# Kernel tuning notes

Hardware: AMD Instinct MI355X
Metric: run time of the kernel (lower is better)

The kernel has to match this reference:

```python
import jax, jax.numpy as jnp
import numpy as np

DIM = 64  # QK head dim, matches init kwarg 'dim'

def setup_inputs() -> dict:
    key = jax.random.key(0)
    kq, kk, kv = jax.random.split(key, 3)
    B, L, C, D, H = 2, 2048, 16, DIM, 64
    query = jax.random.normal(kq, (B, L, C, D), dtype=jnp.float32)
    k_ = jax.random.normal(kk, (B, L, C, D), dtype=jnp.float32)
    value = jax.random.normal(kv, (B, L, C, H), dtype=jnp.float32)
    return {"query": query, "key": k_, "value": value}

def reference(query, key, value):
    scaler = 1.0 / jnp.sqrt(jnp.float32(DIM))
    # score: [b, c, l, m]
    score = jnp.einsum('blcd,bmcd->bclm', query, key) * scaler
    # mask=False, dropout=0 -> identity
    attn = jax.nn.softmax(score, axis=3)
    # out: [b, l, c, h]
    out = jnp.einsum('bmch,bclm->blch', value, attn)
    return out
```

## Files before the change

### kernel.cpp

```cpp
#include <hip/hip_runtime.h>
#include <hip/hip_bf16.h>
#include <stdint.h>

#define B_ 2
#define L_ 2048
#define C_ 16
#define D_ 64
#define H_ 64
#define QBLK 128
#define KVBLK 64
#define NTILES 32
#define NTHREADS 256
#define NHEADS 32
#define TILE_ELEMS 4096
#define TENSOR_ELEMS (NHEADS * NTILES * TILE_ELEMS)

typedef __attribute__((ext_vector_type(8))) short bf16x8;
typedef __attribute__((ext_vector_type(16))) float f32x16;
typedef __attribute__((ext_vector_type(8))) unsigned short u16x8;

__device__ inline unsigned short f2bf(float f) {
  union { float f; unsigned int u; } v; v.f = f;
  unsigned int u = v.u;
  unsigned int r = (u + 0x7FFFu + ((u >> 16) & 1u)) >> 16;
  return (unsigned short)r;
}

__device__ inline float fast_exp2(float x) {
#if __has_builtin(__builtin_amdgcn_exp2f)
  return __builtin_amdgcn_exp2f(x);
#else
  return exp2f(x);
#endif
}

__device__ inline unsigned cvt_pk_bf16(float lo, float hi) {
  unsigned r;
  asm("v_cvt_pk_bf16_f32 %0, %1, %2" : "=v"(r) : "v"(lo), "v"(hi));
  return r;
}

__device__ inline void pl32swap(unsigned &x, unsigned &y) {
#if __has_builtin(__builtin_amdgcn_permlane32_swap)
  auto r = __builtin_amdgcn_permlane32_swap(x, y, false, false);
  x = r[0]; y = r[1];
#else
  asm("v_permlane32_swap_b32 %0, %1" : "+v"(x), "+&v"(y));
#endif
}

__device__ inline float xsum32(float v) {
  unsigned x = __float_as_uint(v), y = x;
  pl32swap(x, y);
  return __uint_as_float(x) + __uint_as_float(y);
}

__global__ __launch_bounds__(256) void prepack_kernel(
    const float* __restrict__ Kg, const float* __restrict__ Vg,
    unsigned short* __restrict__ Kb, unsigned short* __restrict__ Vb) {
  int idx = blockIdx.x * 256 + threadIdx.x;
  if (idx < 524288) {
    int i = idx;
    int lane = i & 63, frag = (i >> 6) & 7, t = (i >> 9) & 31, head = i >> 14;
    int b = head >> 4, c = head & 15;
    int ks = frag >> 1, half = frag & 1;
    int row = half * 32 + (lane & 31);
    int kb = ks * 16 + (lane >> 5) * 8;
    const float* src = Kg + ((size_t)(b * L_ + t * 64 + row) * C_ + c) * D_ + kb;
    float4 a0 = ((const float4*)src)[0];
    float4 a1 = ((const float4*)src)[1];
    u16x8 pk;
    pk[0] = f2bf(a0.x); pk[1] = f2bf(a0.y); pk[2] = f2bf(a0.z); pk[3] = f2bf(a0.w);
    pk[4] = f2bf(a1.x); pk[5] = f2bf(a1.y); pk[6] = f2bf(a1.z); pk[7] = f2bf(a1.w);
    size_t dst = ((((size_t)(head * 32 + t)) * 8 + frag) * 64 + lane) * 8;
    *(u16x8*)&Kb[dst] = pk;
  } else {
    int i = idx - 524288;
    int lane = i & 63, frag = (i >> 6) & 7, t = (i >> 9) & 31, head = i >> 14;
    int b = head >> 4, c = head & 15;
    int m = frag >> 1, half = frag & 1;
    int h = half * 32 + (lane & 31);
    int kv0 = m * 16 + (lane >> 5) * 8;
    const float* src = Vg + ((size_t)(b * L_ + t * 64 + kv0) * C_ + c) * H_ + h;
    u16x8 pv;
#pragma unroll
    for (int j = 0; j < 8; ++j) pv[j] = f2bf(src[(size_t)j * C_ * H_]);
    size_t dst = ((((size_t)(head * 32 + t)) * 8 + frag) * 64 + lane) * 8;
    *(u16x8*)&Vb[dst] = pv;
  }
}

#define TILE_BODY(SC0, SC1, SN0, SN1, T)                                          \
  {                                                                               \
    _Pragma("unroll")                                                             \
    for (int z = 0; z < 16; ++z) { SN0[z] = 0.f; SN1[z] = 0.f; }                  \
    float rst[4];                                                                 \
    bf16x8 pf[4];                                                                 \
    _Pragma("unroll")                                                             \
    for (int i = 0; i < 4; ++i) {                                                 \
      const int be = ((2 * i) & 3) * 4;                                           \
      const int bo = ((2 * i + 1) & 3) * 4;                                       \
      float p0[4], p1[4];                                                         \
      _Pragma("unroll")                                                           \
      for (int r = 0; r < 4; ++r) {                                               \
        float se = (i < 2) ? SC0[be + r] : SC1[be + r];                           \
        float so_ = (i < 2) ? SC0[bo + r] : SC1[bo + r];                          \
        p0[r] = fast_exp2(se);                                                    \
        p1[r] = fast_exp2(so_);                                                   \
      }                                                                           \
      rst[i] = ((p0[0] + p0[1]) + (p0[2] + p0[3])) +                              \
               ((p1[0] + p1[1]) + (p1[2] + p1[3]));                               \
      unsigned x0 = cvt_pk_bf16(p0[0], p0[1]);                                    \
      unsigned x1 = cvt_pk_bf16(p0[2], p0[3]);                                    \
      unsigned y0 = cvt_pk_bf16(p1[0], p1[1]);                                    \
      unsigned y1 = cvt_pk_bf16(p1[2], p1[3]);                                    \
      pl32swap(x0, y0);                                                           \
      pl32swap(x1, y1);                                                           \
      union { unsigned wd[4]; bf16x8 v; } pk_;                                    \
      pk_.wd[0] = x0; pk_.wd[1] = x1; pk_.wd[2] = y0; pk_.wd[3] = y1;             \
      pf[i] = pk_.v;                                                              \
      SN0 = __builtin_amdgcn_mfma_f32_32x32x16_bf16(kf[2 * i], qf[i], SN0, 0, 0, 0);     \
      SN1 = __builtin_amdgcn_mfma_f32_32x32x16_bf16(kf[2 * i + 1], qf[i], SN1, 0, 0, 0); \
    }                                                                             \
    l_own += (rst[0] + rst[1]) + (rst[2] + rst[3]);                               \
    {                                                                             \
      const int tk = ((T) + 2 < NTILES) ? (T) + 2 : NTILES - 1;                   \
      _Pragma("unroll")                                                           \
      for (int f = 0; f < 8; ++f)                                                 \
        kf[f] = *(const bf16x8*)(KbL + (size_t)(tk * 8 + f) * 512);               \
    }                                                                             \
    __builtin_amdgcn_s_setprio(1);                                                \
    _Pragma("unroll")                                                             \
    for (int m = 0; m < 4; ++m) {                                                 \
      o0 = __builtin_amdgcn_mfma_f32_32x32x16_bf16(vf[2 * m], pf[m], o0, 0, 0, 0);       \
      o1 = __builtin_amdgcn_mfma_f32_32x32x16_bf16(vf[2 * m + 1], pf[m], o1, 0, 0, 0);   \
    }                                                                             \
    __builtin_amdgcn_s_setprio(0);                                                \
    {                                                                             \
      const int tv = ((T) + 1 < NTILES) ? (T) + 1 : NTILES - 1;                   \
      _Pragma("unroll")                                                           \
      for (int f = 0; f < 8; ++f)                                                 \
        vf[f] = *(const bf16x8*)(VbL + (size_t)(tv * 8 + f) * 512);               \
    }                                                                             \
  }

__global__ __launch_bounds__(NTHREADS, 2) void attn_fwd_kernel(
    const float* __restrict__ Qg,
    const unsigned short* __restrict__ Kb,
    const unsigned short* __restrict__ Vb,
    float* __restrict__ Og) {
  const int tid  = threadIdx.x;
  const int lane = tid & 63;
  const int w    = tid >> 6;
  const int ql   = lane & 31;
  const int u    = lane >> 5;

  const int bid   = blockIdx.x;
  const int swz   = (bid & 7) * 64 + (bid >> 3);
  const int head  = swz >> 4;
  const int qtile = swz & 15;
  const int b     = head >> 4;
  const int c     = head & 15;
  const int q0    = qtile * QBLK;

  const unsigned short* KbL = Kb + (size_t)head * NTILES * TILE_ELEMS + lane * 8;
  const unsigned short* VbL = Vb + (size_t)head * NTILES * TILE_ELEMS + lane * 8;

  const float sc2 = 0.125f * 1.44269504088896340736f;
  const int qr = q0 + w * 32 + ql;
  const float* qrow = Qg + ((size_t)(b * L_ + qr) * C_ + c) * D_;
  bf16x8 qf[4];
#pragma unroll
  for (int ks = 0; ks < 4; ++ks) {
    float4 a0 = *(const float4*)(qrow + ks * 16 + u * 8);
    float4 a1 = *(const float4*)(qrow + ks * 16 + u * 8 + 4);
    bf16x8 q8;
    q8[0] = (short)f2bf(a0.x * sc2); q8[1] = (short)f2bf(a0.y * sc2);
    q8[2] = (short)f2bf(a0.z * sc2); q8[3] = (short)f2bf(a0.w * sc2);
    q8[4] = (short)f2bf(a1.x * sc2); q8[5] = (short)f2bf(a1.y * sc2);
    q8[6] = (short)f2bf(a1.z * sc2); q8[7] = (short)f2bf(a1.w * sc2);
    qf[ks] = q8;
  }

  f32x16 o0, o1;
#pragma unroll
  for (int i = 0; i < 16; ++i) { o0[i] = 0.f; o1[i] = 0.f; }
  float l_own = 0.f;

  bf16x8 kf[8], vf[8];
#pragma unroll
  for (int f = 0; f < 8; ++f) kf[f] = *(const bf16x8*)(KbL + (size_t)f * 512);
#pragma unroll
  for (int f = 0; f < 8; ++f) vf[f] = *(const bf16x8*)(VbL + (size_t)f * 512);

  f32x16 sA0, sA1, sB0, sB1;
#pragma unroll
  for (int i = 0; i < 16; ++i) { sA0[i] = 0.f; sA1[i] = 0.f; }
  __builtin_amdgcn_s_setprio(1);
#pragma unroll
  for (int ks = 0; ks < 4; ++ks) {
    sA0 = __builtin_amdgcn_mfma_f32_32x32x16_bf16(kf[2 * ks], qf[ks], sA0, 0, 0, 0);
    sA1 = __builtin_amdgcn_mfma_f32_32x32x16_bf16(kf[2 * ks + 1], qf[ks], sA1, 0, 0, 0);
  }
  __builtin_amdgcn_s_setprio(0);
#pragma unroll
  for (int f = 0; f < 8; ++f)
    kf[f] = *(const bf16x8*)(KbL + (size_t)(8 + f) * 512);

  for (int t = 0; t < NTILES; t += 2) {
    TILE_BODY(sA0, sA1, sB0, sB1, t);
    TILE_BODY(sB0, sB1, sA0, sA1, t + 1);
  }

  const float inv = 1.0f / xsum32(l_own);
  float* orow = Og + ((size_t)(b * L_ + qr) * C_ + c) * H_;
#pragma unroll
  for (int rg = 0; rg < 4; ++rg) {
    float4 v0, v1;
    v0.x = o0[rg * 4 + 0] * inv; v0.y = o0[rg * 4 + 1] * inv;
    v0.z = o0[rg * 4 + 2] * inv; v0.w = o0[rg * 4 + 3] * inv;
    v1.x = o1[rg * 4 + 0] * inv; v1.y = o1[rg * 4 + 1] * inv;
    v1.z = o1[rg * 4 + 2] * inv; v1.w = o1[rg * 4 + 3] * inv;
    *(float4*)(orow + 8 * rg + 4 * u) = v0;
    *(float4*)(orow + 32 + 8 * rg + 4 * u) = v1;
  }
}

extern "C" void kernel_launch(void* const* d_in, const int* in_sizes, int n_in,
                              void* d_out, int out_size, void* d_ws, size_t ws_size,
                              hipStream_t stream) {
  const float* Qg = (const float*)d_in[0];
  const float* Kg = (const float*)d_in[1];
  const float* Vg = (const float*)d_in[2];
  float* Og = (float*)d_out;

  unsigned short* Kb = (unsigned short*)d_ws;
  unsigned short* Vb = Kb + (size_t)TENSOR_ELEMS;

  prepack_kernel<<<4096, 256, 0, stream>>>(Kg, Vg, Kb, Vb);

  dim3 grid(NHEADS * (L_ / QBLK));
  dim3 block(NTHREADS);
  attn_fwd_kernel<<<grid, block, 0, stream>>>(Qg, Kb, Vb, Og);
}
```

Baseline: 57.32 us.

## Split KV tiles across wave pairs, reuse K/V fragments for two query groups

Each wave now handles 64 query rows, split into two 32-row groups, over half of the KV tiles (even or odd, chosen by wave parity). Each K/V fragment load is reused for two QK and PV MFMA sets, which halves global K/V reads per block. Partial outputs and row sums are combined through shared memory after a block barrier. The cost is more accumulator registers (four O accumulators), the loss of the previous software pipelining where QK of the next tile overlapped the softmax, and an extra LDS reduction step.

```diff
diff --git a/kernel.cpp b/kernel.cpp
--- a/kernel.cpp
+++ b/kernel.cpp
@@ -90,26 +90,40 @@
   }
 }
 
-#define TILE_BODY(SC0, SC1, SN0, SN1, T)                                          \
+#define GROUP_BODY(OH0, OH1, QF, LWN, IS_LAST, T)                                 \
   {                                                                               \
-    _Pragma("unroll")                                                             \
-    for (int z = 0; z < 16; ++z) { SN0[z] = 0.f; SN1[z] = 0.f; }                  \
+    f32x16 s0, s1;                                                                \
+    _Pragma("unroll")                                                             \
+    for (int z = 0; z < 16; ++z) { s0[z] = 0.f; s1[z] = 0.f; }                    \
+    __builtin_amdgcn_s_setprio(1);                                                \
+    _Pragma("unroll")                                                             \
+    for (int ks = 0; ks < 4; ++ks) {                                              \
+      s0 = __builtin_amdgcn_mfma_f32_32x32x16_bf16(kf[2 * ks], QF[ks], s0, 0, 0, 0);     \
+      s1 = __builtin_amdgcn_mfma_f32_32x32x16_bf16(kf[2 * ks + 1], QF[ks], s1, 0, 0, 0); \
+    }                                                                             \
+    __builtin_amdgcn_s_setprio(0);                                                \
+    if (IS_LAST) {                                                                \
+      const int tk = ((T) + 2 < NTILES) ? (T) + 2 : (T);                          \
+      _Pragma("unroll")                                                           \
+      for (int f = 0; f < 8; ++f)                                                 \
+        kf[f] = *(const bf16x8*)(KbL + (size_t)(tk * 8 + f) * 512);               \
+    }                                                                             \
     float rst[4];                                                                 \
     bf16x8 pf[4];                                                                 \
     _Pragma("unroll")                                                             \
-    for (int i = 0; i < 4; ++i) {                                                 \
-      const int be = ((2 * i) & 3) * 4;                                           \
-      const int bo = ((2 * i + 1) & 3) * 4;                                       \
+    for (int tq = 0; tq < 4; ++tq) {                                              \
+      const int be = ((2 * tq) & 3) * 4;                                          \
+      const int bo = ((2 * tq + 1) & 3) * 4;                                      \
       float p0[4], p1[4];                                                         \
       _Pragma("unroll")                                                           \
       for (int r = 0; r < 4; ++r) {                                               \
-        float se = (i < 2) ? SC0[be + r] : SC1[be + r];                           \
-        float so_ = (i < 2) ? SC0[bo + r] : SC1[bo + r];                          \
+        float se = (tq < 2) ? s0[be + r] : s1[be + r];                            \
+        float so_ = (tq < 2) ? s0[bo + r] : s1[bo + r];                           \
         p0[r] = fast_exp2(se);                                                    \
         p1[r] = fast_exp2(so_);                                                   \
       }                                                                           \
-      rst[i] = ((p0[0] + p0[1]) + (p0[2] + p0[3])) +                              \
-               ((p1[0] + p1[1]) + (p1[2] + p1[3]));                               \
+      rst[tq] = ((p0[0] + p0[1]) + (p0[2] + p0[3])) +                             \
+                ((p1[0] + p1[1]) + (p1[2] + p1[3]));                              \
       unsigned x0 = cvt_pk_bf16(p0[0], p0[1]);                                    \
       unsigned x1 = cvt_pk_bf16(p0[2], p0[3]);                                    \
       unsigned y0 = cvt_pk_bf16(p1[0], p1[1]);                                    \
@@ -118,26 +132,18 @@
       pl32swap(x1, y1);                                                           \
       union { unsigned wd[4]; bf16x8 v; } pk_;                                    \
       pk_.wd[0] = x0; pk_.wd[1] = x1; pk_.wd[2] = y0; pk_.wd[3] = y1;             \
-      pf[i] = pk_.v;                                                              \
-      SN0 = __builtin_amdgcn_mfma_f32_32x32x16_bf16(kf[2 * i], qf[i], SN0, 0, 0, 0);     \
-      SN1 = __builtin_amdgcn_mfma_f32_32x32x16_bf16(kf[2 * i + 1], qf[i], SN1, 0, 0, 0); \
-    }                                                                             \
-    l_own += (rst[0] + rst[1]) + (rst[2] + rst[3]);                               \
-    {                                                                             \
-      const int tk = ((T) + 2 < NTILES) ? (T) + 2 : NTILES - 1;                   \
-      _Pragma("unroll")                                                           \
-      for (int f = 0; f < 8; ++f)                                                 \
-        kf[f] = *(const bf16x8*)(KbL + (size_t)(tk * 8 + f) * 512);               \
-    }                                                                             \
+      pf[tq] = pk_.v;                                                             \
+    }                                                                             \
+    LWN += (rst[0] + rst[1]) + (rst[2] + rst[3]);                                 \
     __builtin_amdgcn_s_setprio(1);                                                \
     _Pragma("unroll")                                                             \
     for (int m = 0; m < 4; ++m) {                                                 \
-      o0 = __builtin_amdgcn_mfma_f32_32x32x16_bf16(vf[2 * m], pf[m], o0, 0, 0, 0);       \
-      o1 = __builtin_amdgcn_mfma_f32_32x32x16_bf16(vf[2 * m + 1], pf[m], o1, 0, 0, 0);   \
+      OH0 = __builtin_amdgcn_mfma_f32_32x32x16_bf16(vf[2 * m], pf[m], OH0, 0, 0, 0);     \
+      OH1 = __builtin_amdgcn_mfma_f32_32x32x16_bf16(vf[2 * m + 1], pf[m], OH1, 0, 0, 0); \
     }                                                                             \
     __builtin_amdgcn_s_setprio(0);                                                \
-    {                                                                             \
-      const int tv = ((T) + 1 < NTILES) ? (T) + 1 : NTILES - 1;                   \
+    if (IS_LAST) {                                                                \
+      const int tv = ((T) + 2 < NTILES) ? (T) + 2 : (T);                          \
       _Pragma("unroll")                                                           \
       for (int f = 0; f < 8; ++f)                                                 \
         vf[f] = *(const bf16x8*)(VbL + (size_t)(tv * 8 + f) * 512);               \
@@ -149,9 +155,14 @@
     const unsigned short* __restrict__ Kb,
     const unsigned short* __restrict__ Vb,
     float* __restrict__ Og) {
+  __shared__ float Osh[2 * 64 * 68];
+  __shared__ float lsh[2 * 2 * 64];
+
   const int tid  = threadIdx.x;
   const int lane = tid & 63;
   const int w    = tid >> 6;
+  const int qw   = w >> 1;
+  const int g    = w & 1;
   const int ql   = lane & 31;
   const int u    = lane >> 5;
 
@@ -161,68 +172,90 @@
   const int qtile = swz & 15;
   const int b     = head >> 4;
   const int c     = head & 15;
-  const int q0    = qtile * QBLK;
+  const int q0    = qtile * QBLK + qw * 64;
 
   const unsigned short* KbL = Kb + (size_t)head * NTILES * TILE_ELEMS + lane * 8;
   const unsigned short* VbL = Vb + (size_t)head * NTILES * TILE_ELEMS + lane * 8;
 
   const float sc2 = 0.125f * 1.44269504088896340736f;
-  const int qr = q0 + w * 32 + ql;
-  const float* qrow = Qg + ((size_t)(b * L_ + qr) * C_ + c) * D_;
-  bf16x8 qf[4];
-#pragma unroll
-  for (int ks = 0; ks < 4; ++ks) {
-    float4 a0 = *(const float4*)(qrow + ks * 16 + u * 8);
-    float4 a1 = *(const float4*)(qrow + ks * 16 + u * 8 + 4);
-    bf16x8 q8;
-    q8[0] = (short)f2bf(a0.x * sc2); q8[1] = (short)f2bf(a0.y * sc2);
-    q8[2] = (short)f2bf(a0.z * sc2); q8[3] = (short)f2bf(a0.w * sc2);
-    q8[4] = (short)f2bf(a1.x * sc2); q8[5] = (short)f2bf(a1.y * sc2);
-    q8[6] = (short)f2bf(a1.z * sc2); q8[7] = (short)f2bf(a1.w * sc2);
-    qf[ks] = q8;
-  }
-
-  f32x16 o0, o1;
-#pragma unroll
-  for (int i = 0; i < 16; ++i) { o0[i] = 0.f; o1[i] = 0.f; }
-  float l_own = 0.f;
+  bf16x8 qf0[4], qf1[4];
+#pragma unroll
+  for (int h = 0; h < 2; ++h) {
+    const int qr = q0 + h * 32 + ql;
+    const float* qrow = Qg + ((size_t)(b * L_ + qr) * C_ + c) * D_;
+#pragma unroll
+    for (int ks = 0; ks < 4; ++ks) {
+      float4 a0 = *(const float4*)(qrow + ks * 16 + u * 8);
+      float4 a1 = *(const float4*)(qrow + ks * 16 + u * 8 + 4);
+      bf16x8 q8;
+      q8[0] = (short)f2bf(a0.x * sc2); q8[1] = (short)f2bf(a0.y * sc2);
+      q8[2] = (short)f2bf(a0.z * sc2); q8[3] = (short)f2bf(a0.w * sc2);
+      q8[4] = (short)f2bf(a1.x * sc2); q8[5] = (short)f2bf(a1.y * sc2);
+      q8[6] = (short)f2bf(a1.z * sc2); q8[7] = (short)f2bf(a1.w * sc2);
+      if (h == 0) qf0[ks] = q8; else qf1[ks] = q8;
+    }
+  }
+
+  f32x16 o00, o01, o10, o11;
+#pragma unroll
+  for (int i = 0; i < 16; ++i) { o00[i] = 0.f; o01[i] = 0.f; o10[i] = 0.f; o11[i] = 0.f; }
+  float l0 = 0.f, l1 = 0.f;
 
   bf16x8 kf[8], vf[8];
 #pragma unroll
-  for (int f = 0; f < 8; ++f) kf[f] = *(const bf16x8*)(KbL + (size_t)f * 512);
-#pragma unroll
-  for (int f = 0; f < 8; ++f) vf[f] = *(const bf16x8*)(VbL + (size_t)f * 512);
-
-  f32x16 sA0, sA1, sB0, sB1;
-#pragma unroll
-  for (int i = 0; i < 16; ++i) { sA0[i] = 0.f; sA1[i] = 0.f; }
-  __builtin_amdgcn_s_setprio(1);
-#pragma unroll
-  for (int ks = 0; ks < 4; ++ks) {
-    sA0 = __builtin_amdgcn_mfma_f32_32x32x16_bf16(kf[2 * ks], qf[ks], sA0, 0, 0, 0);
-    sA1 = __builtin_amdgcn_mfma_f32_32x32x16_bf16(kf[2 * ks + 1], qf[ks], sA1, 0, 0, 0);
-  }
-  __builtin_amdgcn_s_setprio(0);
-#pragma unroll
   for (int f = 0; f < 8; ++f)
-    kf[f] = *(const bf16x8*)(KbL + (size_t)(8 + f) * 512);
-
-  for (int t = 0; t < NTILES; t += 2) {
-    TILE_BODY(sA0, sA1, sB0, sB1, t);
-    TILE_BODY(sB0, sB1, sA0, sA1, t + 1);
-  }
-
-  const float inv = 1.0f / xsum32(l_own);
-  float* orow = Og + ((size_t)(b * L_ + qr) * C_ + c) * H_;
-#pragma unroll
-  for (int rg = 0; rg < 4; ++rg) {
-    float4 v0, v1;
-    v0.x = o0[rg * 4 + 0] * inv; v0.y = o0[rg * 4 + 1] * inv;
-    v0.z = o0[rg * 4 + 2] * inv; v0.w = o0[rg * 4 + 3] * inv;
-    v1.x = o1[rg * 4 + 0] * inv; v1.y = o1[rg * 4 + 1] * inv;
-    v1.z = o1[rg * 4 + 2] * inv; v1.w = o1[rg * 4 + 3] * inv;
-    *(float4*)(orow + 8 * rg + 4 * u) = v0;
-    *(float4*)(orow + 32 + 8 * rg + 4 * u) = v1;
+    kf[f] = *(const bf16x8*)(KbL + (size_t)(g * 8 + f) * 512);
+#pragma unroll
+  for (int f = 0; f < 8; ++f)
+    vf[f] = *(const bf16x8*)(VbL + (size_t)(g * 8 + f) * 512);
+
+  for (int tt = 0; tt < NTILES / 2; ++tt) {
+    const int t = g + 2 * tt;
+    GROUP_BODY(o00, o01, qf0, l0, 0, t);
+    GROUP_BODY(o10, o11, qf1, l1, 1, t);
+  }
+
+  float la0 = xsum32(l0), la1 = xsum32(l1);
+  float* Ow = &Osh[(qw * 64 + lane) * 68];
+  if (g == 1) {
+#pragma unroll
+    for (int rg = 0; rg < 4; ++rg) {
+      *(float4*)(Ow + rg * 4)      = (float4){o00[rg*4+0], o00[rg*4+1], o00[rg*4+2], o00[rg*4+3]};
+      *(float4*)(Ow + 16 + rg * 4) = (float4){o01[rg*4+0], o01[rg*4+1], o01[rg*4+2], o01[rg*4+3]};
+      *(float4*)(Ow + 32 + rg * 4) = (float4){o10[rg*4+0], o10[rg*4+1], o10[rg*4+2], o10[rg*4+3]};
+      *(float4*)(Ow + 48 + rg * 4) = (float4){o11[rg*4+0], o11[rg*4+1], o11[rg*4+2], o11[rg*4+3]};
+    }
+    lsh[(qw * 2 + 0) * 64 + lane] = la0;
+    lsh[(qw * 2 + 1) * 64 + lane] = la1;
+  }
+  __syncthreads();
+  if (g == 0) {
+    const float inv0 = 1.0f / (la0 + lsh[(qw * 2 + 0) * 64 + lane]);
+    const float inv1 = 1.0f / (la1 + lsh[(qw * 2 + 1) * 64 + lane]);
+    const int qr0 = q0 + ql;
+    const int qr1 = q0 + 32 + ql;
+    float* orow0 = Og + ((size_t)(b * L_ + qr0) * C_ + c) * H_;
+    float* orow1 = Og + ((size_t)(b * L_ + qr1) * C_ + c) * H_;
+#pragma unroll
+    for (int rg = 0; rg < 4; ++rg) {
+      float4 a0 = *(const float4*)(Ow + rg * 4);
+      float4 a1 = *(const float4*)(Ow + 16 + rg * 4);
+      float4 a2 = *(const float4*)(Ow + 32 + rg * 4);
+      float4 a3 = *(const float4*)(Ow + 48 + rg * 4);
+      float4 v0, v1, v2, v3;
+      v0.x = (o00[rg*4+0] + a0.x) * inv0; v0.y = (o00[rg*4+1] + a0.y) * inv0;
+      v0.z = (o00[rg*4+2] + a0.z) * inv0; v0.w = (o00[rg*4+3] + a0.w) * inv0;
+      v1.x = (o01[rg*4+0] + a1.x) * inv0; v1.y = (o01[rg*4+1] + a1.y) * inv0;
+      v1.z = (o01[rg*4+2] + a1.z) * inv0; v1.w = (o01[rg*4+3] + a1.w) * inv0;
+      v2.x = (o10[rg*4+0] + a2.x) * inv1; v2.y = (o10[rg*4+1] + a2.y) * inv1;
+      v2.z = (o10[rg*4+2] + a2.z) * inv1; v2.w = (o10[rg*4+3] + a2.w) * inv1;
+      v3.x = (o11[rg*4+0] + a3.x) * inv1; v3.y = (o11[rg*4+1] + a3.y) * inv1;
+      v3.z = (o11[rg*4+2] + a3.z) * inv1; v3.w = (o11[rg*4+3] + a3.w) * inv1;
+      *(float4*)(orow0 + 8 * rg + 4 * u) = v0;
+      *(float4*)(orow0 + 32 + 8 * rg + 4 * u) = v1;
+      *(float4*)(orow1 + 8 * rg + 4 * u) = v2;
+      *(float4*)(orow1 + 32 + 8 * rg + 4 * u) = v3;
+    }
   }
 }
 
```

Result: slower. 75.40 us (+31.5%).
